# Kernel tuning notes

Hardware: AMD Instinct MI355X
Metric: run time of the kernel (lower is better)

## Reference

```python
import jax, jax.numpy as jnp
import numpy as np
from math import sqrt

B, S, E, H = 2, 2048, 1024, 16

def setup_inputs() -> dict:
    key = jax.random.key(0)
    k1, k2, k3, k4, k5 = jax.random.split(key, 5)
    bound_in = 1.0 / sqrt(E)
    return {
        "inputs": jax.random.normal(k1, (B, S, E), dtype=jnp.float32),
        "W_in": jax.random.uniform(k2, (3 * E, E), dtype=jnp.float32, minval=-bound_in, maxval=bound_in),
        "b_in": jax.random.uniform(k3, (3 * E,), dtype=jnp.float32, minval=-bound_in, maxval=bound_in),
        "W_out": jax.random.uniform(k4, (E, E), dtype=jnp.float32, minval=-bound_in, maxval=bound_in),
        "b_out": jax.random.uniform(k5, (E,), dtype=jnp.float32, minval=-bound_in, maxval=bound_in),
    }

def reference(inputs, W_in, b_in, W_out, b_out):
    # Eval-mode forward (dropout is identity when not training).
    b, s, e = inputs.shape
    hd = e // H
    qkv = jnp.einsum('bse,fe->bsf', inputs, W_in) + b_in  # [B,S,3E]
    q, k, v = jnp.split(qkv, 3, axis=-1)
    # [B,S,E] -> [B,H,S,hd]
    to_heads = lambda t: t.reshape(b, s, H, hd).transpose(0, 2, 1, 3)
    q, k, v = to_heads(q), to_heads(k), to_heads(v)
    scores = jnp.einsum('bhqd,bhkd->bhqk', q, k) / jnp.sqrt(jnp.float32(hd))
    causal = jnp.tril(jnp.ones((s, s), dtype=bool))
    scores = jnp.where(causal, scores, -jnp.inf)
    attn = jax.nn.softmax(scores, axis=-1)  # stable max-subtract softmax, same math
    out = jnp.einsum('bhqk,bhkd->bhqd', attn, v)  # [B,H,S,hd]
    out = out.transpose(0, 2, 1, 3).reshape(b, s, e)
    return jnp.einsum('bse,fe->bsf', out, W_out) + b_out
```

## Files before the change

### kernel.cpp

```cpp
#include <hip/hip_runtime.h>
#include <hip/hip_bf16.h>
#include <stdint.h>

#define SS 2048
#define EE 1024
#define HH 16
#define HD 64

#define QSCALE 0.1803368801111137f

typedef __attribute__((ext_vector_type(8))) short short8;
typedef __attribute__((ext_vector_type(4))) float f32x4;

__device__ __forceinline__ short f2bf(float f) {
  union { float f; uint32_t u; } x; x.f = f;
  uint32_t r = x.u + 0x7fffu + ((x.u >> 16) & 1u);
  return (short)(r >> 16);
}

__device__ __forceinline__ uint32_t pk_bf16(float a, float b) {
#if __has_builtin(__builtin_amdgcn_cvt_pk_bf16_f32)
  typedef __attribute__((ext_vector_type(2))) __bf16 bf16x2_t;
  union { bf16x2_t v; uint32_t u; } x;
  x.v = __builtin_amdgcn_cvt_pk_bf16_f32(a, b);
  return x.u;
#else
  return (uint32_t)(uint16_t)f2bf(a) | ((uint32_t)(uint16_t)f2bf(b) << 16);
#endif
}

__device__ __forceinline__ void async_cp16(const void* g, void* l) {
  __builtin_amdgcn_global_load_lds((const __attribute__((address_space(1))) void*)g,
                                   (__attribute__((address_space(3))) void*)l, 16, 0, 0);
}

#define N4_X  1048576
#define N4_W1 786432
#define N4_W2 262144
__global__ __launch_bounds__(256) void cvt_all(
    const float* __restrict__ x, const float* __restrict__ w1,
    const float* __restrict__ w2,
    short* __restrict__ xb, short* __restrict__ w1b, short* __restrict__ w2b)
{
  int i = blockIdx.x * 256 + threadIdx.x;
  const float* src; short* dst; int off;
  if (i < N4_X)            { src = x;  dst = xb;  off = i; }
  else if (i < N4_X+N4_W1) { src = w1; dst = w1b; off = i - N4_X; }
  else                     { src = w2; dst = w2b; off = i - N4_X - N4_W1; }
  float4 v = *(const float4*)&src[(size_t)off * 4];
  uint2 pk;
  pk.x = pk_bf16(v.x, v.y);
  pk.y = pk_bf16(v.z, v.w);
  *(uint2*)&dst[(size_t)off * 4] = pk;
}

template<int MODE>
__global__ __launch_bounds__(256) void gemm_db(
    const short* __restrict__ A, const short* __restrict__ Bw,
    const float* __restrict__ bias,
    float* __restrict__ C,
    short* __restrict__ qw, short* __restrict__ kw, short* __restrict__ vw,
    int M, int N, int K)
{
  __shared__ short smem[(MODE == 1) ? 17408 : 16384];
  const int tid = threadIdx.x;
  const int lane = tid & 63;
  const int wv = tid >> 6;
  const int wm = (wv >> 1) * 64;
  const int wn = (wv & 1) * 64;
  const int t = lane >> 4;
  const int lr = lane & 15;
  const int bm = blockIdx.y * 128;
  const int bn = blockIdx.x * 128;

  f32x4 acc[4][4];
  #pragma unroll
  for (int i = 0; i < 4; ++i)
    #pragma unroll
    for (int j = 0; j < 4; ++j) acc[i][j] = (f32x4){0.f, 0.f, 0.f, 0.f};

  auto stage = [&](int buf, int k0) {
    short* sA = smem + buf * 8192;
    short* sB = smem + buf * 8192 + 4096;
    #pragma unroll
    for (int it = 0; it < 2; ++it) {
      int c = it * 256 + wv * 64 + lane;
      int row = c >> 2;
      int ch = (c & 3) * 8;
      async_cp16(&A[(size_t)(bm + row) * K + k0 + ch],
                 (char*)sA + (size_t)(it * 256 + wv * 64) * 16);
      async_cp16(&Bw[(size_t)(bn + row) * K + k0 + ch],
                 (char*)sB + (size_t)(it * 256 + wv * 64) * 16);
    }
  };

  const int nk = K >> 5;
  stage(0, 0);
  __syncthreads();

  for (int k = 0; k < nk; ++k) {
    if (k + 1 < nk) stage((k + 1) & 1, (k + 1) << 5);
    const short* cA = smem + (k & 1) * 8192;
    const short* cB = smem + (k & 1) * 8192 + 4096;
    short8 af[4], bfr[4];
    #pragma unroll
    for (int i = 0; i < 4; ++i) af[i] = *(const short8*)&cA[(wm + i*16 + lr)*32 + t*8];
    #pragma unroll
    for (int j = 0; j < 4; ++j) bfr[j] = *(const short8*)&cB[(wn + j*16 + lr)*32 + t*8];
    #pragma unroll
    for (int i = 0; i < 4; ++i)
      #pragma unroll
      for (int j = 0; j < 4; ++j)
        acc[i][j] = __builtin_amdgcn_mfma_f32_16x16x32_bf16(af[i], bfr[j], acc[i][j], 0, 0, 0);
    __syncthreads();
  }

  if (MODE == 1 && bn >= 2048) {
    short* vx = smem;
    #pragma unroll
    for (int i = 0; i < 4; ++i) {
      int row0 = wm + i*16 + t*4;
      #pragma unroll
      for (int j = 0; j < 4; ++j) {
        int cl = wn + j*16 + lr;
        float bv = bias[bn + cl];
        #pragma unroll
        for (int r = 0; r < 4; ++r)
          vx[cl*136 + row0 + r] = f2bf(acc[i][j][r] + bv);
      }
    }
    __syncthreads();
    int h0 = (bn - 2048) >> 6;
    int b_ = bm >> 11;
    int s0 = bm & 2047;
    #pragma unroll
    for (int it = 0; it < 8; ++it) {
      int cc = it * 256 + tid;
      int cl = cc >> 4;
      int ck = cc & 15;
      int h = h0 + (cl >> 6);
      int d = cl & 63;
      *(uint4*)&vw[((size_t)(b_*HH + h)*HD + d)*SS + s0 + ck*8] =
          *(const uint4*)&vx[cl*136 + ck*8];
    }
    return;
  }

  #pragma unroll
  for (int i = 0; i < 4; ++i) {
    int row0 = bm + wm + i*16 + t*4;
    #pragma unroll
    for (int j = 0; j < 4; ++j) {
      int col = bn + wn + j*16 + lr;
      float bv = bias[col];
      #pragma unroll
      for (int r = 0; r < 4; ++r) {
        float v = acc[i][j][r] + bv;
        int rr = row0 + r;
        if (MODE == 0) {
          C[(size_t)rr * N + col] = v;
        } else {
          int e = col & 1023;
          int h = e >> 6, d = e & 63;
          int b_ = rr >> 11, s = rr & 2047;
          if (col < 1024)
            qw[((size_t)(b_*HH + h)*SS + s)*HD + d] = f2bf(v * QSCALE);
          else
            kw[((size_t)(b_*HH + h)*SS + s)*HD + d] = f2bf(v);
        }
      }
    }
  }
}

template<int MODE, typename TA>
__global__ __launch_bounds__(256) void gemm_bt(
    const TA* __restrict__ A, const float* __restrict__ Bw,
    const float* __restrict__ bias,
    float* __restrict__ C,
    short* __restrict__ qw, short* __restrict__ kw, short* __restrict__ vw,
    int M, int N, int K)
{
  __shared__ short sA[128*32];
  __shared__ short sB[128*32];
  const int tid = threadIdx.x;
  const int lane = tid & 63;
  const int wv = tid >> 6;
  const int wm = (wv >> 1) * 64;
  const int wn = (wv & 1) * 64;
  const int t = lane >> 4;
  const int lr = lane & 15;
  const int bm = blockIdx.y * 128;
  const int bn = blockIdx.x * 128;

  f32x4 acc[4][4];
  #pragma unroll
  for (int i = 0; i < 4; ++i)
    #pragma unroll
    for (int j = 0; j < 4; ++j) acc[i][j] = (f32x4){0.f, 0.f, 0.f, 0.f};

  for (int k0 = 0; k0 < K; k0 += 32) {
    __syncthreads();
    if constexpr (sizeof(TA) == 4) {
      #pragma unroll
      for (int it = 0; it < 4; ++it) {
        int c = it * 256 + tid;
        int row = c >> 3, ch = (c & 7) * 4;
        float4 va = *(const float4*)&A[(size_t)(bm + row)*K + k0 + ch];
        uint2 pk; pk.x = pk_bf16(va.x, va.y); pk.y = pk_bf16(va.z, va.w);
        *(uint2*)&sA[row*32 + ch] = pk;
      }
    } else {
      #pragma unroll
      for (int it = 0; it < 2; ++it) {
        int c = it * 256 + tid;
        int row = c >> 2, ch = (c & 3) * 8;
        *(uint4*)&sA[row*32 + ch] = *(const uint4*)&A[(size_t)(bm + row)*K + k0 + ch];
      }
    }
    #pragma unroll
    for (int it = 0; it < 4; ++it) {
      int c = it * 256 + tid;
      int row = c >> 3, ch = (c & 7) * 4;
      float4 vb = *(const float4*)&Bw[(size_t)(bn + row)*K + k0 + ch];
      uint2 pk; pk.x = pk_bf16(vb.x, vb.y); pk.y = pk_bf16(vb.z, vb.w);
      *(uint2*)&sB[row*32 + ch] = pk;
    }
    __syncthreads();
    short8 af[4], bfr[4];
    #pragma unroll
    for (int i = 0; i < 4; ++i) af[i] = *(const short8*)&sA[(wm + i*16 + lr)*32 + t*8];
    #pragma unroll
    for (int j = 0; j < 4; ++j) bfr[j] = *(const short8*)&sB[(wn + j*16 + lr)*32 + t*8];
    #pragma unroll
    for (int i = 0; i < 4; ++i)
      #pragma unroll
      for (int j = 0; j < 4; ++j)
        acc[i][j] = __builtin_amdgcn_mfma_f32_16x16x32_bf16(af[i], bfr[j], acc[i][j], 0, 0, 0);
  }

  #pragma unroll
  for (int i = 0; i < 4; ++i) {
    int row0 = bm + wm + i*16 + t*4;
    #pragma unroll
    for (int j = 0; j < 4; ++j) {
      int col = bn + wn + j*16 + lr;
      float bv = bias[col];
      #pragma unroll
      for (int r = 0; r < 4; ++r) {
        float v = acc[i][j][r] + bv;
        int rr = row0 + r;
        if (MODE == 0) {
          C[(size_t)rr * N + col] = v;
        } else {
          int which = col >> 10;
          int e = col & 1023;
          int h = e >> 6, d = e & 63;
          int b_ = rr >> 11, s = rr & 2047;
          if (which == 0)
            qw[((size_t)(b_*HH + h)*SS + s)*HD + d] = f2bf(v * QSCALE);
          else if (which == 1)
            kw[((size_t)(b_*HH + h)*SS + s)*HD + d] = f2bf(v);
          else
            vw[((size_t)(b_*HH + h)*HD + d)*SS + s] = f2bf(v);
        }
      }
    }
  }
}

__global__ __launch_bounds__(512) void attn_kernel(
    const short* __restrict__ Q, const short* __restrict__ K,
    const short* __restrict__ Vt, short* __restrict__ O)
{
  __shared__ short sK[2][128*64];
  __shared__ short sV[2][64*128];
  __shared__ short sP[8][16*128];
  const int tid = threadIdx.x;
  const int lane = tid & 63;
  const int w = tid >> 6;
  const int t = lane >> 4;
  const int lr = lane & 15;
  const int pairIdx = blockIdx.x >> 5;
  const int bh = blockIdx.x & 31;
  const int b = bh >> 4, h = bh & 15;
  const short* Qb = Q  + (size_t)bh * SS * HD;
  const short* Kb = K  + (size_t)bh * SS * HD;
  const short* Vb = Vt + (size_t)bh * HD * SS;
  short* sPw = sP[w];

  auto stage = [&](int buf, int kb) {
    #pragma unroll
    for (int it2 = 0; it2 < 2; ++it2) {
      int s = it2 * 512 + tid;
      int krow = s >> 3;
      int kcc = (s & 7) ^ (krow & 7);
      async_cp16(&Kb[(size_t)(kb + krow) * HD + kcc * 8],
                 (char*)sK[buf] + (size_t)(it2 * 512 + w * 64) * 16);
      int d = s >> 4;
      int vcc = (s & 15) ^ (d & 15);
      async_cp16(&Vb[(size_t)d * SS + kb + vcc * 8],
                 (char*)sV[buf] + (size_t)(it2 * 512 + w * 64) * 16);
    }
  };

  #pragma unroll 1
  for (int phase = 0; phase < 2; ++phase) {
    const int qt = phase ? (15 - pairIdx) : pairIdx;
    const int qrow0 = qt * 128 + w * 16;
    const int niter = qt + 1;

    short8 qf[2];
    #pragma unroll
    for (int st = 0; st < 2; ++st)
      qf[st] = *(const short8*)&Qb[(size_t)(qrow0 + lr) * HD + st*32 + t*8];

    f32x4 o[4];
    #pragma unroll
    for (int jd = 0; jd < 4; ++jd) o[jd] = (f32x4){0.f, 0.f, 0.f, 0.f};
    float m = -1e30f, l = 0.f;

    stage(0, 0);
    __syncthreads();
    int cur = 0;

    #pragma unroll 1
    for (int it = 0; it < niter; ++it) {
      const int kb = it * 128;
      if (it + 1 < niter) stage(cur ^ 1, kb + 128);

      const short* sKc = sK[cur];
      const short* sVc = sV[cur];

      f32x4 sc[8];
      #pragma unroll
      for (int c = 0; c < 8; ++c) sc[c] = (f32x4){0.f,0.f,0.f,0.f};
      #pragma unroll
      for (int c = 0; c < 8; ++c) {
        int krow = c*16 + lr;
        #pragma unroll
        for (int st = 0; st < 2; ++st) {
          int slot = krow*8 + ((st*4 + t) ^ (krow & 7));
          short8 kf = *(const short8*)&sKc[slot*8];
          sc[c] = __builtin_amdgcn_mfma_f32_16x16x32_bf16(kf, qf[st], sc[c], 0, 0, 0);
        }
      }

      if (it == niter - 1) {
        int qg = qrow0 + lr;
        #pragma unroll
        for (int c = 0; c < 8; ++c)
          #pragma unroll
          for (int r = 0; r < 4; ++r)
            if (kb + c*16 + t*4 + r > qg) sc[c][r] = -1e30f;
      }

      float mx = sc[0][0];
      #pragma unroll
      for (int c = 0; c < 8; ++c)
        #pragma unroll
        for (int r = 0; r < 4; ++r) mx = fmaxf(mx, sc[c][r]);
      mx = fmaxf(mx, __shfl_xor(mx, 16));
      mx = fmaxf(mx, __shfl_xor(mx, 32));

      float mn = fmaxf(m, mx);
      float alpha = exp2f(m - mn);
      m = mn;
      float rs = 0.f;
      #pragma unroll
      for (int c = 0; c < 8; ++c)
        #pragma unroll
        for (int r = 0; r < 4; ++r) {
          sc[c][r] = exp2f(sc[c][r] - mn);
          rs += sc[c][r];
        }
      rs += __shfl_xor(rs, 16);
      rs += __shfl_xor(rs, 32);
      l = l * alpha + rs;

      float alr[4];
      #pragma unroll
      for (int r = 0; r < 4; ++r) alr[r] = __shfl(alpha, 20*t + r);
      #pragma unroll
      for (int jd = 0; jd < 4; ++jd)
        #pragma unroll
        for (int r = 0; r < 4; ++r) o[jd][r] *= alr[r];

      #pragma unroll
      for (int c = 0; c < 8; ++c) {
        uint2 pk2;
        pk2.x = pk_bf16(sc[c][0], sc[c][1]);
        pk2.y = pk_bf16(sc[c][2], sc[c][3]);
        int chunk = 2*c + (t >> 1);
        int slot = lr*16 + (chunk ^ lr);
        *(uint2*)&sPw[slot*8 + (t & 1)*4] = pk2;
      }
      #pragma unroll
      for (int f = 0; f < 4; ++f) {
        int pslot = lr*16 + ((f*4 + t) ^ lr);
        short8 pf = *(const short8*)&sPw[pslot*8];
        #pragma unroll
        for (int jd = 0; jd < 4; ++jd) {
          int d = jd*16 + lr;
          int vslot = d*16 + ((f*4 + t) ^ (d & 15));
          short8 vf = *(const short8*)&sVc[vslot*8];
          o[jd] = __builtin_amdgcn_mfma_f32_16x16x32_bf16(pf, vf, o[jd], 0, 0, 0);
        }
      }

      __syncthreads();
      cur ^= 1;
    }

    float linv[4];
    #pragma unroll
    for (int r = 0; r < 4; ++r) linv[r] = 1.0f / __shfl(l, 20*t + r);
    #pragma unroll
    for (int jd = 0; jd < 4; ++jd)
      #pragma unroll
      for (int r = 0; r < 4; ++r) {
        int qrow = qrow0 + t*4 + r;
        int d = jd*16 + lr;
        O[((size_t)(b * SS + qrow)) * EE + h * HD + d] = f2bf(o[jd][r] * linv[r]);
      }
  }
}

extern "C" void kernel_launch(void* const* d_in, const int* in_sizes, int n_in,
                              void* d_out, int out_size, void* d_ws, size_t ws_size,
                              hipStream_t stream) {
  const float* X     = (const float*)d_in[0];
  const float* W_in  = (const float*)d_in[1];
  const float* b_in  = (const float*)d_in[2];
  const float* W_out = (const float*)d_in[3];
  const float* b_out = (const float*)d_in[4];
  float* out = (float*)d_out;

  char* ws = (char*)d_ws;
  const size_t MB = 1024 * 1024;
  const int M = 2 * SS;

  if (ws_size >= 48 * MB) {
    short* Xb   = (short*)(ws);
    short* Wb1  = (short*)(ws + 8  * MB);
    short* Wb2  = (short*)(ws + 14 * MB);
    short* q_ws = (short*)(ws + 16 * MB);
    short* k_ws = (short*)(ws + 24 * MB);
    short* v_ws = (short*)(ws + 32 * MB);
    short* attn = (short*)(ws + 40 * MB);

    cvt_all<<<8192, 256, 0, stream>>>(X, W_in, W_out, Xb, Wb1, Wb2);
    gemm_db<1><<<dim3(24, 32), 256, 0, stream>>>(
        Xb, Wb1, b_in, nullptr, q_ws, k_ws, v_ws, M, 3 * EE, EE);
    attn_kernel<<<dim3(256), 512, 0, stream>>>(q_ws, k_ws, v_ws, attn);
    gemm_db<0><<<dim3(8, 32), 256, 0, stream>>>(
        attn, Wb2, b_out, out, nullptr, nullptr, nullptr, M, EE, EE);
  } else {
    short* q_ws = (short*)(ws);
    short* k_ws = (short*)(ws + 8  * MB);
    short* v_ws = (short*)(ws + 16 * MB);
    short* attn = (short*)(ws + 24 * MB);

    gemm_bt<1, float><<<dim3(24, 32), 256, 0, stream>>>(
        X, W_in, b_in, nullptr, q_ws, k_ws, v_ws, M, 3 * EE, EE);
    attn_kernel<<<dim3(256), 512, 0, stream>>>(q_ws, k_ws, v_ws, attn);
    gemm_bt<0, short><<<dim3(8, 32), 256, 0, stream>>>(
        attn, W_out, b_out, out, nullptr, nullptr, nullptr, M, EE, EE);
  }
}
```

Measured before the change: 195.3 us.

## Share K/V tile loads across paired query tiles in one causal sweep

Each block used to walk its two paired query tiles (p and 15-p) one after another, staging K/V for each. Now both tiles' state lives in registers at once and a single K/V sweep of 16-p blocks is made. Each staged tile feeds the B tile and, while in range, the A tile. This removes the repeated global loads and syncs for the first p+1 K/V blocks, at the cost of more registers (two sets of Q fragments and accumulators) and possibly lower occupancy or spills.

```diff
diff --git a/kernel.cpp b/kernel.cpp
--- a/kernel.cpp
+++ b/kernel.cpp
@@ -281,13 +281,16 @@
   const int w = tid >> 6;
   const int t = lane >> 4;
   const int lr = lane & 15;
-  const int pairIdx = blockIdx.x >> 5;
+  const int p = blockIdx.x >> 5;
   const int bh = blockIdx.x & 31;
   const int b = bh >> 4, h = bh & 15;
   const short* Qb = Q  + (size_t)bh * SS * HD;
   const short* Kb = K  + (size_t)bh * SS * HD;
   const short* Vb = Vt + (size_t)bh * HD * SS;
   short* sPw = sP[w];
+
+  const int qrow0A = p * 128 + w * 16;
+  const int qrow0B = (15 - p) * 128 + w * 16;
 
   auto stage = [&](int buf, int kb) {
     #pragma unroll
@@ -304,114 +307,119 @@
     }
   };
 
-  #pragma unroll 1
-  for (int phase = 0; phase < 2; ++phase) {
-    const int qt = phase ? (15 - pairIdx) : pairIdx;
-    const int qrow0 = qt * 128 + w * 16;
-    const int niter = qt + 1;
-
-    short8 qf[2];
-    #pragma unroll
-    for (int st = 0; st < 2; ++st)
-      qf[st] = *(const short8*)&Qb[(size_t)(qrow0 + lr) * HD + st*32 + t*8];
-
-    f32x4 o[4];
-    #pragma unroll
-    for (int jd = 0; jd < 4; ++jd) o[jd] = (f32x4){0.f, 0.f, 0.f, 0.f};
-    float m = -1e30f, l = 0.f;
-
-    stage(0, 0);
-    __syncthreads();
-    int cur = 0;
-
-    #pragma unroll 1
-    for (int it = 0; it < niter; ++it) {
-      const int kb = it * 128;
-      if (it + 1 < niter) stage(cur ^ 1, kb + 128);
-
-      const short* sKc = sK[cur];
-      const short* sVc = sV[cur];
-
-      f32x4 sc[8];
-      #pragma unroll
-      for (int c = 0; c < 8; ++c) sc[c] = (f32x4){0.f,0.f,0.f,0.f};
-      #pragma unroll
-      for (int c = 0; c < 8; ++c) {
-        int krow = c*16 + lr;
-        #pragma unroll
-        for (int st = 0; st < 2; ++st) {
-          int slot = krow*8 + ((st*4 + t) ^ (krow & 7));
-          short8 kf = *(const short8*)&sKc[slot*8];
-          sc[c] = __builtin_amdgcn_mfma_f32_16x16x32_bf16(kf, qf[st], sc[c], 0, 0, 0);
-        }
-      }
-
-      if (it == niter - 1) {
-        int qg = qrow0 + lr;
-        #pragma unroll
-        for (int c = 0; c < 8; ++c)
-          #pragma unroll
-          for (int r = 0; r < 4; ++r)
-            if (kb + c*16 + t*4 + r > qg) sc[c][r] = -1e30f;
-      }
-
-      float mx = sc[0][0];
+  short8 qfA[2], qfB[2];
+  #pragma unroll
+  for (int st = 0; st < 2; ++st) {
+    qfA[st] = *(const short8*)&Qb[(size_t)(qrow0A + lr) * HD + st*32 + t*8];
+    qfB[st] = *(const short8*)&Qb[(size_t)(qrow0B + lr) * HD + st*32 + t*8];
+  }
+
+  f32x4 oA[4], oB[4];
+  #pragma unroll
+  for (int jd = 0; jd < 4; ++jd) {
+    oA[jd] = (f32x4){0.f, 0.f, 0.f, 0.f};
+    oB[jd] = (f32x4){0.f, 0.f, 0.f, 0.f};
+  }
+  float mA = -1e30f, lA = 0.f, mB = -1e30f, lB = 0.f;
+
+  auto process = [&](const short* sKc, const short* sVc, const short8* qf,
+                     f32x4* o, float& m, float& l, int kb, bool diag, int qrow0) {
+    f32x4 sc[8];
+    #pragma unroll
+    for (int c = 0; c < 8; ++c) sc[c] = (f32x4){0.f,0.f,0.f,0.f};
+    #pragma unroll
+    for (int c = 0; c < 8; ++c) {
+      int krow = c*16 + lr;
+      #pragma unroll
+      for (int st = 0; st < 2; ++st) {
+        int slot = krow*8 + ((st*4 + t) ^ (krow & 7));
+        short8 kf = *(const short8*)&sKc[slot*8];
+        sc[c] = __builtin_amdgcn_mfma_f32_16x16x32_bf16(kf, qf[st], sc[c], 0, 0, 0);
+      }
+    }
+    if (diag) {
+      int qg = qrow0 + lr;
       #pragma unroll
       for (int c = 0; c < 8; ++c)
         #pragma unroll
-        for (int r = 0; r < 4; ++r) mx = fmaxf(mx, sc[c][r]);
-      mx = fmaxf(mx, __shfl_xor(mx, 16));
-      mx = fmaxf(mx, __shfl_xor(mx, 32));
-
-      float mn = fmaxf(m, mx);
-      float alpha = exp2f(m - mn);
-      m = mn;
-      float rs = 0.f;
-      #pragma unroll
-      for (int c = 0; c < 8; ++c)
-        #pragma unroll
-        for (int r = 0; r < 4; ++r) {
-          sc[c][r] = exp2f(sc[c][r] - mn);
-          rs += sc[c][r];
-        }
-      rs += __shfl_xor(rs, 16);
-      rs += __shfl_xor(rs, 32);
-      l = l * alpha + rs;
-
-      float alr[4];
-      #pragma unroll
-      for (int r = 0; r < 4; ++r) alr[r] = __shfl(alpha, 20*t + r);
-      #pragma unroll
-      for (int jd = 0; jd < 4; ++jd)
-        #pragma unroll
-        for (int r = 0; r < 4; ++r) o[jd][r] *= alr[r];
-
-      #pragma unroll
-      for (int c = 0; c < 8; ++c) {
-        uint2 pk2;
-        pk2.x = pk_bf16(sc[c][0], sc[c][1]);
-        pk2.y = pk_bf16(sc[c][2], sc[c][3]);
-        int chunk = 2*c + (t >> 1);
-        int slot = lr*16 + (chunk ^ lr);
-        *(uint2*)&sPw[slot*8 + (t & 1)*4] = pk2;
-      }
-      #pragma unroll
-      for (int f = 0; f < 4; ++f) {
-        int pslot = lr*16 + ((f*4 + t) ^ lr);
-        short8 pf = *(const short8*)&sPw[pslot*8];
-        #pragma unroll
-        for (int jd = 0; jd < 4; ++jd) {
-          int d = jd*16 + lr;
-          int vslot = d*16 + ((f*4 + t) ^ (d & 15));
-          short8 vf = *(const short8*)&sVc[vslot*8];
-          o[jd] = __builtin_amdgcn_mfma_f32_16x16x32_bf16(pf, vf, o[jd], 0, 0, 0);
-        }
-      }
-
-      __syncthreads();
-      cur ^= 1;
-    }
-
+        for (int r = 0; r < 4; ++r)
+          if (kb + c*16 + t*4 + r > qg) sc[c][r] = -1e30f;
+    }
+    float mx = sc[0][0];
+    #pragma unroll
+    for (int c = 0; c < 8; ++c)
+      #pragma unroll
+      for (int r = 0; r < 4; ++r) mx = fmaxf(mx, sc[c][r]);
+    mx = fmaxf(mx, __shfl_xor(mx, 16));
+    mx = fmaxf(mx, __shfl_xor(mx, 32));
+
+    float mn = fmaxf(m, mx);
+    float alpha = exp2f(m - mn);
+    m = mn;
+    float rs = 0.f;
+    #pragma unroll
+    for (int c = 0; c < 8; ++c)
+      #pragma unroll
+      for (int r = 0; r < 4; ++r) {
+        sc[c][r] = exp2f(sc[c][r] - mn);
+        rs += sc[c][r];
+      }
+    rs += __shfl_xor(rs, 16);
+    rs += __shfl_xor(rs, 32);
+    l = l * alpha + rs;
+
+    float alr[4];
+    #pragma unroll
+    for (int r = 0; r < 4; ++r) alr[r] = __shfl(alpha, 20*t + r);
+    #pragma unroll
+    for (int jd = 0; jd < 4; ++jd)
+      #pragma unroll
+      for (int r = 0; r < 4; ++r) o[jd][r] *= alr[r];
+
+    #pragma unroll
+    for (int c = 0; c < 8; ++c) {
+      uint2 pk2;
+      pk2.x = pk_bf16(sc[c][0], sc[c][1]);
+      pk2.y = pk_bf16(sc[c][2], sc[c][3]);
+      int chunk = 2*c + (t >> 1);
+      int slot = lr*16 + (chunk ^ lr);
+      *(uint2*)&sPw[slot*8 + (t & 1)*4] = pk2;
+    }
+    #pragma unroll
+    for (int f = 0; f < 4; ++f) {
+      int pslot = lr*16 + ((f*4 + t) ^ lr);
+      short8 pf = *(const short8*)&sPw[pslot*8];
+      #pragma unroll
+      for (int jd = 0; jd < 4; ++jd) {
+        int d = jd*16 + lr;
+        int vslot = d*16 + ((f*4 + t) ^ (d & 15));
+        short8 vf = *(const short8*)&sVc[vslot*8];
+        o[jd] = __builtin_amdgcn_mfma_f32_16x16x32_bf16(pf, vf, o[jd], 0, 0, 0);
+      }
+    }
+  };
+
+  const int niter = 16 - p;
+  const int nA = p + 1;
+
+  stage(0, 0);
+  __syncthreads();
+  int cur = 0;
+
+  #pragma unroll 1
+  for (int it = 0; it < niter; ++it) {
+    const int kb = it * 128;
+    if (it + 1 < niter) stage(cur ^ 1, kb + 128);
+    const short* sKc = sK[cur];
+    const short* sVc = sV[cur];
+    process(sKc, sVc, qfB, oB, mB, lB, kb, it == niter - 1, qrow0B);
+    if (it < nA)
+      process(sKc, sVc, qfA, oA, mA, lA, kb, it == nA - 1, qrow0A);
+    __syncthreads();
+    cur ^= 1;
+  }
+
+  auto writeout = [&](const f32x4* o, float l, int qrow0) {
     float linv[4];
     #pragma unroll
     for (int r = 0; r < 4; ++r) linv[r] = 1.0f / __shfl(l, 20*t + r);
@@ -423,7 +431,9 @@
         int d = jd*16 + lr;
         O[((size_t)(b * SS + qrow)) * EE + h * HD + d] = f2bf(o[jd][r] * linv[r]);
       }
-  }
+  };
+  writeout(oB, lB, qrow0B);
+  writeout(oA, lA, qrow0A);
 }
 
 extern "C" void kernel_launch(void* const* d_in, const int* in_sizes, int n_in,
```

Measured after the change: 202.1 us. 3.5% more time.

## Split attention into one block per query tile and pass P through shuffles

Applied to the files above, without the earlier changes.

The attention kernel now launches 512 blocks, one per query tile, instead of 256 blocks that each ran two paired tiles in sequence. The probability tile P is moved between lanes with cross-lane shuffles instead of a trip through shared memory. The PV MFMA operands are swapped so the output is laid out per row, which removes the alpha and l broadcast shuffles and allows packed 8-byte output stores. Dropping the sP buffer lowers LDS use and could raise occupancy, but the causal work is no longer balanced within each block and each block does more shuffle work.

```diff
diff --git a/kernel.cpp b/kernel.cpp
--- a/kernel.cpp
+++ b/kernel.cpp
@@ -275,19 +275,19 @@
 {
   __shared__ short sK[2][128*64];
   __shared__ short sV[2][64*128];
-  __shared__ short sP[8][16*128];
   const int tid = threadIdx.x;
   const int lane = tid & 63;
   const int w = tid >> 6;
   const int t = lane >> 4;
   const int lr = lane & 15;
-  const int pairIdx = blockIdx.x >> 5;
-  const int bh = blockIdx.x & 31;
+  const int blk = blockIdx.x;
+  const int qt = (blk < 256) ? (blk >> 5) : (15 - ((blk - 256) >> 5));
+  const int bh = blk & 31;
   const int b = bh >> 4, h = bh & 15;
   const short* Qb = Q  + (size_t)bh * SS * HD;
   const short* Kb = K  + (size_t)bh * SS * HD;
   const short* Vb = Vt + (size_t)bh * HD * SS;
-  short* sPw = sP[w];
+  const int qrow0 = qt * 128 + w * 16;
 
   auto stage = [&](int buf, int kb) {
     #pragma unroll
@@ -304,125 +304,126 @@
     }
   };
 
+  short8 qf[2];
+  #pragma unroll
+  for (int st = 0; st < 2; ++st)
+    qf[st] = *(const short8*)&Qb[(size_t)(qrow0 + lr) * HD + st*32 + t*8];
+
+  f32x4 o[4];
+  #pragma unroll
+  for (int jd = 0; jd < 4; ++jd) o[jd] = (f32x4){0.f, 0.f, 0.f, 0.f};
+  float m = -1e30f, l = 0.f;
+
+  const int srcA = 32 * (t & 1) + lr;
+  const int srcB = srcA + 16;
+  const bool hi = (t >> 1) != 0;
+
+  const int niter = qt + 1;
+  stage(0, 0);
+  __syncthreads();
+  int cur = 0;
+
   #pragma unroll 1
-  for (int phase = 0; phase < 2; ++phase) {
-    const int qt = phase ? (15 - pairIdx) : pairIdx;
-    const int qrow0 = qt * 128 + w * 16;
-    const int niter = qt + 1;
-
-    short8 qf[2];
-    #pragma unroll
-    for (int st = 0; st < 2; ++st)
-      qf[st] = *(const short8*)&Qb[(size_t)(qrow0 + lr) * HD + st*32 + t*8];
-
-    f32x4 o[4];
-    #pragma unroll
-    for (int jd = 0; jd < 4; ++jd) o[jd] = (f32x4){0.f, 0.f, 0.f, 0.f};
-    float m = -1e30f, l = 0.f;
-
-    stage(0, 0);
-    __syncthreads();
-    int cur = 0;
-
-    #pragma unroll 1
-    for (int it = 0; it < niter; ++it) {
-      const int kb = it * 128;
-      if (it + 1 < niter) stage(cur ^ 1, kb + 128);
-
-      const short* sKc = sK[cur];
-      const short* sVc = sV[cur];
-
-      f32x4 sc[8];
-      #pragma unroll
-      for (int c = 0; c < 8; ++c) sc[c] = (f32x4){0.f,0.f,0.f,0.f};
-      #pragma unroll
-      for (int c = 0; c < 8; ++c) {
-        int krow = c*16 + lr;
-        #pragma unroll
-        for (int st = 0; st < 2; ++st) {
-          int slot = krow*8 + ((st*4 + t) ^ (krow & 7));
-          short8 kf = *(const short8*)&sKc[slot*8];
-          sc[c] = __builtin_amdgcn_mfma_f32_16x16x32_bf16(kf, qf[st], sc[c], 0, 0, 0);
-        }
-      }
-
-      if (it == niter - 1) {
-        int qg = qrow0 + lr;
-        #pragma unroll
-        for (int c = 0; c < 8; ++c)
-          #pragma unroll
-          for (int r = 0; r < 4; ++r)
-            if (kb + c*16 + t*4 + r > qg) sc[c][r] = -1e30f;
-      }
-
-      float mx = sc[0][0];
+  for (int it = 0; it < niter; ++it) {
+    const int kb = it * 128;
+    if (it + 1 < niter) stage(cur ^ 1, kb + 128);
+    const short* sKc = sK[cur];
+    const short* sVc = sV[cur];
+
+    f32x4 sc[8];
+    #pragma unroll
+    for (int c = 0; c < 8; ++c) sc[c] = (f32x4){0.f,0.f,0.f,0.f};
+    #pragma unroll
+    for (int c = 0; c < 8; ++c) {
+      int krow = c*16 + lr;
+      #pragma unroll
+      for (int st = 0; st < 2; ++st) {
+        int slot = krow*8 + ((st*4 + t) ^ (krow & 7));
+        short8 kf = *(const short8*)&sKc[slot*8];
+        sc[c] = __builtin_amdgcn_mfma_f32_16x16x32_bf16(kf, qf[st], sc[c], 0, 0, 0);
+      }
+    }
+
+    if (it == niter - 1) {
+      int qg = qrow0 + lr;
       #pragma unroll
       for (int c = 0; c < 8; ++c)
         #pragma unroll
-        for (int r = 0; r < 4; ++r) mx = fmaxf(mx, sc[c][r]);
-      mx = fmaxf(mx, __shfl_xor(mx, 16));
-      mx = fmaxf(mx, __shfl_xor(mx, 32));
-
-      float mn = fmaxf(m, mx);
-      float alpha = exp2f(m - mn);
-      m = mn;
-      float rs = 0.f;
-      #pragma unroll
-      for (int c = 0; c < 8; ++c)
-        #pragma unroll
-        for (int r = 0; r < 4; ++r) {
-          sc[c][r] = exp2f(sc[c][r] - mn);
-          rs += sc[c][r];
-        }
-      rs += __shfl_xor(rs, 16);
-      rs += __shfl_xor(rs, 32);
-      l = l * alpha + rs;
-
-      float alr[4];
-      #pragma unroll
-      for (int r = 0; r < 4; ++r) alr[r] = __shfl(alpha, 20*t + r);
-      #pragma unroll
-      for (int jd = 0; jd < 4; ++jd)
-        #pragma unroll
-        for (int r = 0; r < 4; ++r) o[jd][r] *= alr[r];
-
-      #pragma unroll
-      for (int c = 0; c < 8; ++c) {
-        uint2 pk2;
-        pk2.x = pk_bf16(sc[c][0], sc[c][1]);
-        pk2.y = pk_bf16(sc[c][2], sc[c][3]);
-        int chunk = 2*c + (t >> 1);
-        int slot = lr*16 + (chunk ^ lr);
-        *(uint2*)&sPw[slot*8 + (t & 1)*4] = pk2;
-      }
-      #pragma unroll
-      for (int f = 0; f < 4; ++f) {
-        int pslot = lr*16 + ((f*4 + t) ^ lr);
-        short8 pf = *(const short8*)&sPw[pslot*8];
-        #pragma unroll
-        for (int jd = 0; jd < 4; ++jd) {
-          int d = jd*16 + lr;
-          int vslot = d*16 + ((f*4 + t) ^ (d & 15));
-          short8 vf = *(const short8*)&sVc[vslot*8];
-          o[jd] = __builtin_amdgcn_mfma_f32_16x16x32_bf16(pf, vf, o[jd], 0, 0, 0);
-        }
-      }
-
-      __syncthreads();
-      cur ^= 1;
-    }
-
-    float linv[4];
-    #pragma unroll
-    for (int r = 0; r < 4; ++r) linv[r] = 1.0f / __shfl(l, 20*t + r);
+        for (int r = 0; r < 4; ++r)
+          if (kb + c*16 + t*4 + r > qg) sc[c][r] = -1e30f;
+    }
+
+    float mx = sc[0][0];
+    #pragma unroll
+    for (int c = 0; c < 8; ++c)
+      #pragma unroll
+      for (int r = 0; r < 4; ++r) mx = fmaxf(mx, sc[c][r]);
+    mx = fmaxf(mx, __shfl_xor(mx, 16));
+    mx = fmaxf(mx, __shfl_xor(mx, 32));
+
+    float mn = fmaxf(m, mx);
+    float alpha = exp2f(m - mn);
+    m = mn;
+    float rs = 0.f;
+    #pragma unroll
+    for (int c = 0; c < 8; ++c)
+      #pragma unroll
+      for (int r = 0; r < 4; ++r) {
+        sc[c][r] = exp2f(sc[c][r] - mn);
+        rs += sc[c][r];
+      }
+    rs += __shfl_xor(rs, 16);
+    rs += __shfl_xor(rs, 32);
+    l = l * alpha + rs;
+
     #pragma unroll
     for (int jd = 0; jd < 4; ++jd)
       #pragma unroll
-      for (int r = 0; r < 4; ++r) {
-        int qrow = qrow0 + t*4 + r;
+      for (int r = 0; r < 4; ++r) o[jd][r] *= alpha;
+
+    uint32_t ux[8], uy[8];
+    #pragma unroll
+    for (int c = 0; c < 8; ++c) {
+      ux[c] = pk_bf16(sc[c][0], sc[c][1]);
+      uy[c] = pk_bf16(sc[c][2], sc[c][3]);
+    }
+
+    #pragma unroll
+    for (int f = 0; f < 4; ++f) {
+      uint32_t x0 = __shfl(ux[2*f],     srcA);
+      uint32_t y0 = __shfl(uy[2*f],     srcA);
+      uint32_t x1 = __shfl(ux[2*f + 1], srcA);
+      uint32_t y1 = __shfl(uy[2*f + 1], srcA);
+      uint32_t X0 = __shfl(ux[2*f],     srcB);
+      uint32_t Y0 = __shfl(uy[2*f],     srcB);
+      uint32_t X1 = __shfl(ux[2*f + 1], srcB);
+      uint32_t Y1 = __shfl(uy[2*f + 1], srcB);
+      union { uint32_t u[4]; short8 s8; } pf;
+      pf.u[0] = hi ? x1 : x0;
+      pf.u[1] = hi ? y1 : y0;
+      pf.u[2] = hi ? X1 : X0;
+      pf.u[3] = hi ? Y1 : Y0;
+      #pragma unroll
+      for (int jd = 0; jd < 4; ++jd) {
         int d = jd*16 + lr;
-        O[((size_t)(b * SS + qrow)) * EE + h * HD + d] = f2bf(o[jd][r] * linv[r]);
-      }
+        int vslot = d*16 + ((f*4 + t) ^ (d & 15));
+        short8 vf = *(const short8*)&sVc[vslot*8];
+        o[jd] = __builtin_amdgcn_mfma_f32_16x16x32_bf16(vf, pf.s8, o[jd], 0, 0, 0);
+      }
+    }
+
+    __syncthreads();
+    cur ^= 1;
+  }
+
+  float linv = 1.0f / l;
+  size_t rowoff = ((size_t)(b * SS + qrow0 + lr)) * EE + h * HD;
+  #pragma unroll
+  for (int jd = 0; jd < 4; ++jd) {
+    uint2 pw;
+    pw.x = pk_bf16(o[jd][0] * linv, o[jd][1] * linv);
+    pw.y = pk_bf16(o[jd][2] * linv, o[jd][3] * linv);
+    *(uint2*)&O[rowoff + jd*16 + t*4] = pw;
   }
 }
 
@@ -452,7 +453,7 @@
     cvt_all<<<8192, 256, 0, stream>>>(X, W_in, W_out, Xb, Wb1, Wb2);
     gemm_db<1><<<dim3(24, 32), 256, 0, stream>>>(
         Xb, Wb1, b_in, nullptr, q_ws, k_ws, v_ws, M, 3 * EE, EE);
-    attn_kernel<<<dim3(256), 512, 0, stream>>>(q_ws, k_ws, v_ws, attn);
+    attn_kernel<<<dim3(512), 512, 0, stream>>>(q_ws, k_ws, v_ws, attn);
     gemm_db<0><<<dim3(8, 32), 256, 0, stream>>>(
         attn, Wb2, b_out, out, nullptr, nullptr, nullptr, M, EE, EE);
   } else {
@@ -463,7 +464,7 @@
 
     gemm_bt<1, float><<<dim3(24, 32), 256, 0, stream>>>(
         X, W_in, b_in, nullptr, q_ws, k_ws, v_ws, M, 3 * EE, EE);
-    attn_kernel<<<dim3(256), 512, 0, stream>>>(q_ws, k_ws, v_ws, attn);
+    attn_kernel<<<dim3(512), 512, 0, stream>>>(q_ws, k_ws, v_ws, attn);
     gemm_bt<0, short><<<dim3(8, 32), 256, 0, stream>>>(
         attn, W_out, b_out, out, nullptr, nullptr, nullptr, M, EE, EE);
   }
```

Result: no change. 197.3 us (+1.0%).
